# Optimization experiments

Measured on AMD Instinct MI355X. Metric: run time of the kernel, lower is better.

## Reference

```python
import jax, jax.numpy as jnp
import numpy as np

D_MODEL = 2048
NUM_HEADS = 16
D_K = D_MODEL // NUM_HEADS


def setup_inputs() -> dict:
    key = jax.random.key(0)
    ks = jax.random.split(key, 12)
    B, S, D = 2, 2048, D_MODEL
    s = 1.0 / np.sqrt(D)
    return {
        "q": jax.random.normal(ks[0], (B, S, D), jnp.float32),
        "k": jax.random.normal(ks[1], (B, S, D), jnp.float32),
        "v": jax.random.normal(ks[2], (B, S, D), jnp.float32),
        "Wq": jax.random.normal(ks[3], (D, D), jnp.float32) * s,
        "bq": jax.random.normal(ks[4], (D,), jnp.float32) * 0.01,
        "Wk": jax.random.normal(ks[5], (D, D), jnp.float32) * s,
        "bk": jax.random.normal(ks[6], (D,), jnp.float32) * 0.01,
        "Wv": jax.random.normal(ks[7], (D, D), jnp.float32) * s,
        "bv": jax.random.normal(ks[8], (D,), jnp.float32) * 0.01,
        "Wo": jax.random.normal(ks[9], (D, D), jnp.float32) * s,
        "bo": jax.random.normal(ks[10], (D,), jnp.float32) * 0.01,
    }


def reference(q, k, v, Wq, bq, Wk, bk, Wv, bv, Wo, bo):
    B, S, D = q.shape
    H, dk = NUM_HEADS, D_K

    def proj(x, W, b):
        # Linear then split heads -> [B, H, S, dk]
        y = jnp.einsum('bsd,df->bsf', x, W) + b
        return y.reshape(B, -1, H, dk).transpose(0, 2, 1, 3)

    Q = proj(q, Wq, bq)
    K = proj(k, Wk, bk)
    V = proj(v, Wv, bv)

    scores = jnp.einsum('bhqd,bhkd->bhqk', Q, K) / jnp.sqrt(jnp.float32(dk))
    attn = jax.nn.softmax(scores, axis=-1)  # dropout is identity (eval)
    out = jnp.einsum('bhqk,bhkd->bhqd', attn, V)
    out = out.transpose(0, 2, 1, 3).reshape(B, -1, D)
    return jnp.einsum('bsd,df->bsf', out, Wo) + bo
```

## Files before the change

kernel.cpp:

```cpp
#include <hip/hip_runtime.h>
#include <hip/hip_bf16.h>
#include <stdint.h>

typedef float  f32x4  __attribute__((ext_vector_type(4)));
typedef float  f32x16 __attribute__((ext_vector_type(16)));
typedef short  s16x8  __attribute__((ext_vector_type(8)));

#define D_MODEL 2048
#define NHEADS  16
#define DK      128
#define BATCH   2
#define SEQ     2048
#define MROWS   (BATCH*SEQ)

__device__ __forceinline__ unsigned short f2bf(float f) {
  union { float f; unsigned int u; } v; v.f = f;
  unsigned int r = v.u + 0x7FFFu + ((v.u >> 16) & 1u);
  return (unsigned short)(r >> 16);
}

__device__ __forceinline__ unsigned int packbf(float lo, float hi) {
  return (unsigned int)f2bf(lo) | ((unsigned int)f2bf(hi) << 16);
}

__device__ __forceinline__ unsigned int packbf_c(float lo, float hi) {
  __hip_bfloat16 l = __float2bfloat16(lo);
  __hip_bfloat16 h = __float2bfloat16(hi);
  unsigned short lu, hu;
  __builtin_memcpy(&lu, &l, 2);
  __builtin_memcpy(&hu, &h, 2);
  return (unsigned int)lu | ((unsigned int)hu << 16);
}

__device__ __forceinline__ void async16(const void* g, void* l) {
  __builtin_amdgcn_global_load_lds(
      (const __attribute__((address_space(1))) unsigned int*)g,
      (__attribute__((address_space(3))) unsigned int*)l,
      16, 0, 0);
}

__global__ __launch_bounds__(256) void f2b3_kernel(const float* __restrict__ q,
                                                   const float* __restrict__ k,
                                                   const float* __restrict__ v,
                                                   unsigned short* __restrict__ qb,
                                                   unsigned short* __restrict__ kb,
                                                   unsigned short* __restrict__ vb) {
  const float* s; unsigned short* d;
  switch (blockIdx.y) {
    case 0:  s = q; d = qb; break;
    case 1:  s = k; d = kb; break;
    default: s = v; d = vb; break;
  }
  int i = blockIdx.x * 256 + threadIdx.x;
  const float4* s4 = (const float4*)s;
  float4 a = s4[2*i];
  float4 b = s4[2*i+1];
  s16x8 o;
  o[0] = (short)f2bf(a.x); o[1] = (short)f2bf(a.y);
  o[2] = (short)f2bf(a.z); o[3] = (short)f2bf(a.w);
  o[4] = (short)f2bf(b.x); o[5] = (short)f2bf(b.y);
  o[6] = (short)f2bf(b.z); o[7] = (short)f2bf(b.w);
  *(s16x8*)(d + 8*(size_t)i) = o;
}

__global__ __launch_bounds__(256) void wtrans_kernel(const float* __restrict__ Wq,
                                                     const float* __restrict__ Wk,
                                                     const float* __restrict__ Wv,
                                                     const float* __restrict__ Wo,
                                                     unsigned short* __restrict__ WqT,
                                                     unsigned short* __restrict__ WkT,
                                                     unsigned short* __restrict__ WvT,
                                                     unsigned short* __restrict__ WoT) {
  const float* W; unsigned short* Wt;
  switch (blockIdx.z) {
    case 0:  W = Wq; Wt = WqT; break;
    case 1:  W = Wk; Wt = WkT; break;
    case 2:  W = Wv; Wt = WvT; break;
    default: W = Wo; Wt = WoT; break;
  }
  __shared__ float tl[32][33];
  int x = threadIdx.x, y = threadIdx.y;
  int n0 = blockIdx.x * 32, k0 = blockIdx.y * 32;
  #pragma unroll
  for (int j = 0; j < 32; j += 8)
    tl[y + j][x] = W[(size_t)(k0 + y + j) * D_MODEL + n0 + x];
  __syncthreads();
  #pragma unroll
  for (int j = 0; j < 32; j += 8)
    Wt[(size_t)(n0 + y + j) * D_MODEL + k0 + x] = f2bf(tl[x][y + j]);
}

__global__ __launch_bounds__(256) void gemm_bt(const unsigned short* __restrict__ A,
                                               const unsigned short* __restrict__ Bt,
                                               const float* __restrict__ bias,
                                               void* __restrict__ Cout,
                                               int M, int N, int K,
                                               int mode, float scale) {
  __shared__ unsigned short As[128*32];
  __shared__ unsigned short Bs[128*32];
  const int t  = threadIdx.x;
  const int l  = t & 63, w = t >> 6;
  const int wr = w >> 1, wc = w & 1;
  const int m0 = blockIdx.y * 128, n0 = blockIdx.x * 128;
  const int lr = l & 15, lg = l >> 4;

  f32x4 acc[4][4] = {};

  for (int k0 = 0; k0 < K; k0 += 32) {
    __syncthreads();
    #pragma unroll
    for (int i = 0; i < 2; ++i) {
      int c    = t + 256*i;
      int row  = c >> 2;
      int col8 = (c & 3) * 8;
      async16(A  + (size_t)(m0 + row)*K + k0 + col8, (char*)As + c*16);
      async16(Bt + (size_t)(n0 + row)*K + k0 + col8, (char*)Bs + c*16);
    }
    asm volatile("s_waitcnt vmcnt(0)" ::: "memory");
    __syncthreads();

    s16x8 af[4], bfr[4];
    #pragma unroll
    for (int m = 0; m < 4; ++m)
      af[m] = *(const s16x8*)&As[(wr*64 + m*16 + lr)*32 + 8*lg];
    #pragma unroll
    for (int n = 0; n < 4; ++n)
      bfr[n] = *(const s16x8*)&Bs[(wc*64 + n*16 + lr)*32 + 8*lg];
    #pragma unroll
    for (int m = 0; m < 4; ++m)
      #pragma unroll
      for (int n = 0; n < 4; ++n)
        acc[m][n] = __builtin_amdgcn_mfma_f32_16x16x32_bf16(af[m], bfr[n], acc[m][n], 0, 0, 0);
  }

  if (mode == 0) {
    float* C = (float*)Cout;
    #pragma unroll
    for (int n = 0; n < 4; ++n) {
      int col = n0 + wc*64 + n*16 + lr;
      float bv = bias[col];
      #pragma unroll
      for (int m = 0; m < 4; ++m) {
        int rowb = m0 + wr*64 + m*16 + lg*4;
        #pragma unroll
        for (int r = 0; r < 4; ++r)
          C[(size_t)(rowb + r)*N + col] = (acc[m][n][r] + bv) * scale;
      }
    }
  } else {
    unsigned short* C = (unsigned short*)Cout;
    #pragma unroll
    for (int n = 0; n < 4; ++n) {
      int col = n0 + wc*64 + n*16 + lr;
      float bv = bias[col];
      int h = col >> 7, dkk = col & 127;
      #pragma unroll
      for (int m = 0; m < 4; ++m) {
        int rowb = m0 + wr*64 + m*16 + lg*4;
        #pragma unroll
        for (int r = 0; r < 4; ++r) {
          int row = rowb + r;
          int b = row >> 11, s = row & 2047;
          C[((size_t)((b*NHEADS + h)*SEQ + s))*DK + dkk] = f2bf((acc[m][n][r] + bv) * scale);
        }
      }
    }
  }
}

__global__ __launch_bounds__(256, 2) void attn_kernel(const unsigned short* __restrict__ Q,
                                                      const unsigned short* __restrict__ K,
                                                      const unsigned short* __restrict__ V,
                                                      unsigned short* __restrict__ O) {
  #define BUFSZ (64*256 + 128*144)
  __shared__ char lds[2*BUFSZ];

  const int t  = threadIdx.x;
  const int l  = t & 63, w = t >> 6;
  const int q_ = l & 31, hi = l >> 5;
  const int bh = blockIdx.y;
  const int b  = bh >> 4, h = bh & 15;
  const int q0 = blockIdx.x * 128;

  const unsigned short* Qp = Q + (size_t)bh * SEQ * DK;
  const unsigned short* Kp = K + (size_t)bh * SEQ * DK;
  const unsigned short* Vp = V + (size_t)bh * SEQ * DK;

  const int qrow = q0 + w*32 + q_;
  s16x8 aq[8];
  #pragma unroll
  for (int kk = 0; kk < 8; ++kk)
    aq[kk] = *(const s16x8*)(Qp + (size_t)qrow*DK + kk*16 + hi*8);

  f32x16 accO[4] = {};
  float m = -INFINITY, L = 0.f;

  const int vp_ = t & 31;
  const int vd0 = (t >> 5) * 8;

  s16x8 va0, vb0, va1, vb1;

  {
    char* KlN = lds;
    #pragma unroll
    for (int i = 0; i < 4; ++i) {
      int c   = t + 256*i;
      int row = c >> 4;
      int sb  = ((c & 15) << 4) ^ ((row & 15) << 4);
      async16((const char*)(Kp + (size_t)row*DK) + sb, KlN + c*16);
    }
    va0 = *(const s16x8*)(Vp + (size_t)(2*vp_    )*DK + vd0);
    vb0 = *(const s16x8*)(Vp + (size_t)(2*vp_ + 1)*DK + vd0);
    va1 = *(const s16x8*)(Vp + (size_t)(2*vp_    )*DK + vd0 + 64);
    vb1 = *(const s16x8*)(Vp + (size_t)(2*vp_ + 1)*DK + vd0 + 64);
  }

  for (int tt = 0; tt < SEQ/64; ++tt) {
    char*           Kl = lds + (tt & 1)*BUFSZ;
    unsigned short* Vt = (unsigned short*)(Kl + 64*256);

    asm volatile("s_waitcnt vmcnt(0)" ::: "memory");
    #pragma unroll
    for (int j = 0; j < 8; ++j) {
      unsigned int pk0 = (unsigned int)(unsigned short)va0[j]
                       | ((unsigned int)(unsigned short)vb0[j] << 16);
      *(unsigned int*)&Vt[(vd0 + j)*72 + 2*vp_] = pk0;
      unsigned int pk1 = (unsigned int)(unsigned short)va1[j]
                       | ((unsigned int)(unsigned short)vb1[j] << 16);
      *(unsigned int*)&Vt[(vd0 + 64 + j)*72 + 2*vp_] = pk1;
    }
    asm volatile("s_waitcnt lgkmcnt(0)" ::: "memory");
    __syncthreads();

    if (tt + 1 < SEQ/64) {
      int   kvn = (tt + 1) * 64;
      char* KlN = lds + ((tt & 1) ^ 1)*BUFSZ;
      #pragma unroll
      for (int i = 0; i < 4; ++i) {
        int c   = t + 256*i;
        int row = c >> 4;
        int sb  = ((c & 15) << 4) ^ ((row & 15) << 4);
        async16((const char*)(Kp + (size_t)(kvn + row)*DK) + sb, KlN + c*16);
      }
      va0 = *(const s16x8*)(Vp + (size_t)(kvn + 2*vp_    )*DK + vd0);
      vb0 = *(const s16x8*)(Vp + (size_t)(kvn + 2*vp_ + 1)*DK + vd0);
      va1 = *(const s16x8*)(Vp + (size_t)(kvn + 2*vp_    )*DK + vd0 + 64);
      vb1 = *(const s16x8*)(Vp + (size_t)(kvn + 2*vp_ + 1)*DK + vd0 + 64);
    }

    f32x16 S0 = {}, S1 = {};
    #pragma unroll
    for (int t2 = 0; t2 < 2; ++t2) {
      int krow = t2*32 + q_;
      const char* kb = Kl + krow*256;
      int swz = (krow & 15) << 4;
      #pragma unroll
      for (int kk = 0; kk < 8; ++kk) {
        s16x8 kf = *(const s16x8*)(kb + ((kk*32 + hi*16) ^ swz));
        if (t2 == 0) S0 = __builtin_amdgcn_mfma_f32_32x32x16_bf16(kf, aq[kk], S0, 0, 0, 0);
        else         S1 = __builtin_amdgcn_mfma_f32_32x32x16_bf16(kf, aq[kk], S1, 0, 0, 0);
      }
    }

    f32x16 mx;
    #pragma unroll
    for (int r = 0; r < 16; ++r) mx[r] = fmaxf(S0[r], S1[r]);
    float m8_[8];
    #pragma unroll
    for (int r = 0; r < 8; ++r) m8_[r] = fmaxf(mx[r], mx[r+8]);
    float m4a = fmaxf(m8_[0], m8_[4]), m4b = fmaxf(m8_[1], m8_[5]);
    float m4c = fmaxf(m8_[2], m8_[6]), m4d = fmaxf(m8_[3], m8_[7]);
    float pmax = fmaxf(fmaxf(m4a, m4b), fmaxf(m4c, m4d));
    pmax = fmaxf(pmax, __shfl_xor(pmax, 32, 64));

    if (!__all(pmax <= m + 11.0f)) {
      float mnew = fmaxf(m, pmax);
      float corr = exp2f(m - mnew);
      m = mnew;
      L *= corr;
      #pragma unroll
      for (int sub = 0; sub < 4; ++sub)
        #pragma unroll
        for (int r = 0; r < 16; ++r) accO[sub][r] *= corr;
    }

    float rs0 = 0.f, rs1 = 0.f, rs2 = 0.f, rs3 = 0.f;
    #pragma unroll
    for (int r = 0; r < 4; ++r) {
      float a0 = exp2f(S0[r]    - m); S0[r]    = a0; rs0 += a0;
      float a1 = exp2f(S0[r+4]  - m); S0[r+4]  = a1; rs1 += a1;
      float a2 = exp2f(S0[r+8]  - m); S0[r+8]  = a2; rs2 += a2;
      float a3 = exp2f(S0[r+12] - m); S0[r+12] = a3; rs3 += a3;
      float b0 = exp2f(S1[r]    - m); S1[r]    = b0; rs0 += b0;
      float b1 = exp2f(S1[r+4]  - m); S1[r+4]  = b1; rs1 += b1;
      float b2 = exp2f(S1[r+8]  - m); S1[r+8]  = b2; rs2 += b2;
      float b3 = exp2f(S1[r+12] - m); S1[r+12] = b3; rs3 += b3;
    }
    float rs = (rs0 + rs1) + (rs2 + rs3);
    rs += __shfl_xor(rs, 32, 64);
    L += rs;

    s16x8 PB[4];
    #pragma unroll
    for (int t2 = 0; t2 < 2; ++t2) {
      #pragma unroll
      for (int half = 0; half < 2; ++half) {
        int bse = half*8;
        unsigned int pkA01, pkA23, pkB01, pkB23;
        if (t2 == 0) {
          pkA01 = packbf_c(S0[bse+0], S0[bse+1]);
          pkA23 = packbf_c(S0[bse+2], S0[bse+3]);
          pkB01 = packbf_c(S0[bse+4], S0[bse+5]);
          pkB23 = packbf_c(S0[bse+6], S0[bse+7]);
        } else {
          pkA01 = packbf_c(S1[bse+0], S1[bse+1]);
          pkA23 = packbf_c(S1[bse+2], S1[bse+3]);
          pkB01 = packbf_c(S1[bse+4], S1[bse+5]);
          pkB23 = packbf_c(S1[bse+6], S1[bse+7]);
        }
        unsigned int xA01 = __shfl_xor(pkA01, 32, 64);
        unsigned int xA23 = __shfl_xor(pkA23, 32, 64);
        unsigned int xB01 = __shfl_xor(pkB01, 32, 64);
        unsigned int xB23 = __shfl_xor(pkB23, 32, 64);
        union { unsigned int u[4]; s16x8 v; } f;
        f.u[0] = hi ? xB01 : pkA01;
        f.u[1] = hi ? xB23 : pkA23;
        f.u[2] = hi ? pkB01 : xA01;
        f.u[3] = hi ? pkB23 : xA23;
        PB[t2*2 + half] = f.v;
      }
    }

    #pragma unroll
    for (int sub = 0; sub < 4; ++sub) {
      const char* vb2 = (const char*)Vt + (size_t)(sub*32 + q_)*144 + hi*16;
      #pragma unroll
      for (int kk = 0; kk < 4; ++kk) {
        s16x8 vf = *(const s16x8*)(vb2 + kk*32);
        accO[sub] = __builtin_amdgcn_mfma_f32_32x32x16_bf16(vf, PB[kk], accO[sub], 0, 0, 0);
      }
    }
  }

  __syncthreads();
  unsigned short* Ob = (unsigned short*)lds + (size_t)w*4096;
  float inv = 1.0f / L;
  #pragma unroll
  for (int sub = 0; sub < 4; ++sub)
    #pragma unroll
    for (int j = 0; j < 8; ++j) {
      unsigned int pw = packbf_c(accO[sub][2*j]*inv, accO[sub][2*j+1]*inv);
      int dv = sub*32 + (j&1)*2 + ((j>>1)*8) + 4*hi;
      *(unsigned int*)((char*)Ob + q_*256 + ((dv*2) ^ ((q_ & 15) << 4))) = pw;
    }
  asm volatile("s_waitcnt lgkmcnt(0)" ::: "memory");
  size_t gbase = ((size_t)(b*SEQ + q0 + w*32 + q_))*D_MODEL + h*DK;
  #pragma unroll
  for (int p = 0; p < 8; ++p) {
    int chunk = hi + 2*p;
    s16x8 ov = *(const s16x8*)((char*)Ob + q_*256 + ((chunk*16) ^ ((q_ & 15) << 4)));
    *(s16x8*)(O + gbase + chunk*8) = ov;
  }
  #undef BUFSZ
}

extern "C" void kernel_launch(void* const* d_in, const int* in_sizes, int n_in,
                              void* d_out, int out_size, void* d_ws, size_t ws_size,
                              hipStream_t stream) {
  const float* q  = (const float*)d_in[0];
  const float* k  = (const float*)d_in[1];
  const float* v  = (const float*)d_in[2];
  const float* Wq = (const float*)d_in[3];
  const float* bq = (const float*)d_in[4];
  const float* Wk = (const float*)d_in[5];
  const float* bk = (const float*)d_in[6];
  const float* Wv = (const float*)d_in[7];
  const float* bv = (const float*)d_in[8];
  const float* Wo = (const float*)d_in[9];
  const float* bo = (const float*)d_in[10];
  float* out = (float*)d_out;

  char* ws = (char*)d_ws;
  const size_t SZT = (size_t)MROWS * D_MODEL * 2;
  const size_t SZW = (size_t)D_MODEL * D_MODEL * 2;

  unsigned short* qb  = (unsigned short*)(ws);
  unsigned short* kb  = (unsigned short*)(ws + SZT);
  unsigned short* vb  = (unsigned short*)(ws + 2*SZT);
  unsigned short* WqT = (unsigned short*)(ws + 3*SZT);
  unsigned short* WkT = (unsigned short*)(ws + 3*SZT + SZW);
  unsigned short* WvT = (unsigned short*)(ws + 3*SZT + 2*SZW);
  unsigned short* WoT = (unsigned short*)(ws + 3*SZT + 3*SZW);
  unsigned short* Qh  = (unsigned short*)(ws + 3*SZT + 4*SZW);
  unsigned short* Kh  = (unsigned short*)(ws + 4*SZT + 4*SZW);
  unsigned short* Vh  = (unsigned short*)(ws + 5*SZT + 4*SZW);
  unsigned short* Oc  = qb;

  const int n8 = MROWS * D_MODEL / 8;
  f2b3_kernel<<<dim3(n8/256, 3), 256, 0, stream>>>(q, k, v, qb, kb, vb);
  wtrans_kernel<<<dim3(64, 64, 4), dim3(32, 8), 0, stream>>>(Wq, Wk, Wv, Wo, WqT, WkT, WvT, WoT);

  const float qscale = 0.1275174308f;
  gemm_bt<<<dim3(16, 32), 256, 0, stream>>>(qb, WqT, bq, Qh, MROWS, D_MODEL, D_MODEL, 1, qscale);
  gemm_bt<<<dim3(16, 32), 256, 0, stream>>>(kb, WkT, bk, Kh, MROWS, D_MODEL, D_MODEL, 1, 1.0f);
  gemm_bt<<<dim3(16, 32), 256, 0, stream>>>(vb, WvT, bv, Vh, MROWS, D_MODEL, D_MODEL, 1, 1.0f);

  attn_kernel<<<dim3(SEQ/128, BATCH*NHEADS), 256, 0, stream>>>(Qh, Kh, Vh, Oc);

  gemm_bt<<<dim3(16, 32), 256, 0, stream>>>(Oc, WoT, bo, out, MROWS, D_MODEL, D_MODEL, 0, 1.0f);
}
```

Measured before the change: 374.5 us.

## Double-buffer GEMM tiles; single-buffer attention K/V for higher occupancy

The projection GEMM now double-buffers its A/B LDS tiles, issuing the async loads for the next K-slice before computing the current one, so global loads overlap the MFMAs. The attention kernel moves the other way: it drops its double-buffered K/V staging for a single buffer and raises its launch bound from 2 to 4 blocks per CU, relying on occupancy rather than in-kernel prefetch to hide latency. This trades explicit overlap in attention for more resident waves, which may help or hurt depending on register pressure and LDS limits.

```diff
diff --git a/kernel.cpp b/kernel.cpp
--- a/kernel.cpp
+++ b/kernel.cpp
@@ -17,10 +17,6 @@
   union { float f; unsigned int u; } v; v.f = f;
   unsigned int r = v.u + 0x7FFFu + ((v.u >> 16) & 1u);
   return (unsigned short)(r >> 16);
-}
-
-__device__ __forceinline__ unsigned int packbf(float lo, float hi) {
-  return (unsigned int)f2bf(lo) | ((unsigned int)f2bf(hi) << 16);
 }
 
 __device__ __forceinline__ unsigned int packbf_c(float lo, float hi) {
@@ -96,41 +92,51 @@
                                                void* __restrict__ Cout,
                                                int M, int N, int K,
                                                int mode, float scale) {
-  __shared__ unsigned short As[128*32];
-  __shared__ unsigned short Bs[128*32];
+  __shared__ unsigned short As[2][128*32];
+  __shared__ unsigned short Bs[2][128*32];
   const int t  = threadIdx.x;
   const int l  = t & 63, w = t >> 6;
   const int wr = w >> 1, wc = w & 1;
   const int m0 = blockIdx.y * 128, n0 = blockIdx.x * 128;
   const int lr = l & 15, lg = l >> 4;
 
+  const int c0row = t >> 2, c0col = (t & 3) * 8;
+  const int c1row = (t + 256) >> 2, c1col = ((t + 256) & 3) * 8;
+
+  async16(A  + (size_t)(m0 + c0row)*K + c0col, (char*)As[0] + t*16);
+  async16(Bt + (size_t)(n0 + c0row)*K + c0col, (char*)Bs[0] + t*16);
+  async16(A  + (size_t)(m0 + c1row)*K + c1col, (char*)As[0] + (t+256)*16);
+  async16(Bt + (size_t)(n0 + c1row)*K + c1col, (char*)Bs[0] + (t+256)*16);
+  asm volatile("s_waitcnt vmcnt(0)" ::: "memory");
+  __syncthreads();
+
   f32x4 acc[4][4] = {};
 
   for (int k0 = 0; k0 < K; k0 += 32) {
-    __syncthreads();
-    #pragma unroll
-    for (int i = 0; i < 2; ++i) {
-      int c    = t + 256*i;
-      int row  = c >> 2;
-      int col8 = (c & 3) * 8;
-      async16(A  + (size_t)(m0 + row)*K + k0 + col8, (char*)As + c*16);
-      async16(Bt + (size_t)(n0 + row)*K + k0 + col8, (char*)Bs + c*16);
-    }
+    const int cur = (k0 >> 5) & 1;
+    if (k0 + 32 < K) {
+      const int kn = k0 + 32;
+      async16(A  + (size_t)(m0 + c0row)*K + kn + c0col, (char*)As[cur^1] + t*16);
+      async16(Bt + (size_t)(n0 + c0row)*K + kn + c0col, (char*)Bs[cur^1] + t*16);
+      async16(A  + (size_t)(m0 + c1row)*K + kn + c1col, (char*)As[cur^1] + (t+256)*16);
+      async16(Bt + (size_t)(n0 + c1row)*K + kn + c1col, (char*)Bs[cur^1] + (t+256)*16);
+    }
+
+    s16x8 af[4], bfr[4];
+    #pragma unroll
+    for (int m = 0; m < 4; ++m)
+      af[m] = *(const s16x8*)&As[cur][(wr*64 + m*16 + lr)*32 + 8*lg];
+    #pragma unroll
+    for (int n = 0; n < 4; ++n)
+      bfr[n] = *(const s16x8*)&Bs[cur][(wc*64 + n*16 + lr)*32 + 8*lg];
+    #pragma unroll
+    for (int m = 0; m < 4; ++m)
+      #pragma unroll
+      for (int n = 0; n < 4; ++n)
+        acc[m][n] = __builtin_amdgcn_mfma_f32_16x16x32_bf16(af[m], bfr[n], acc[m][n], 0, 0, 0);
+
     asm volatile("s_waitcnt vmcnt(0)" ::: "memory");
     __syncthreads();
-
-    s16x8 af[4], bfr[4];
-    #pragma unroll
-    for (int m = 0; m < 4; ++m)
-      af[m] = *(const s16x8*)&As[(wr*64 + m*16 + lr)*32 + 8*lg];
-    #pragma unroll
-    for (int n = 0; n < 4; ++n)
-      bfr[n] = *(const s16x8*)&Bs[(wc*64 + n*16 + lr)*32 + 8*lg];
-    #pragma unroll
-    for (int m = 0; m < 4; ++m)
-      #pragma unroll
-      for (int n = 0; n < 4; ++n)
-        acc[m][n] = __builtin_amdgcn_mfma_f32_16x16x32_bf16(af[m], bfr[n], acc[m][n], 0, 0, 0);
   }
 
   if (mode == 0) {
@@ -168,12 +174,13 @@
   }
 }
 
-__global__ __launch_bounds__(256, 2) void attn_kernel(const unsigned short* __restrict__ Q,
+__global__ __launch_bounds__(256, 4) void attn_kernel(const unsigned short* __restrict__ Q,
                                                       const unsigned short* __restrict__ K,
                                                       const unsigned short* __restrict__ V,
                                                       unsigned short* __restrict__ O) {
-  #define BUFSZ (64*256 + 128*144)
-  __shared__ char lds[2*BUFSZ];
+  __shared__ char lds[64*256 + 128*144];
+  unsigned short* Kl = (unsigned short*)lds;
+  unsigned short* Vt = (unsigned short*)(lds + 64*256);
 
   const int t  = threadIdx.x;
   const int l  = t & 63, w = t >> 6;
@@ -198,61 +205,35 @@
   const int vp_ = t & 31;
   const int vd0 = (t >> 5) * 8;
 
-  s16x8 va0, vb0, va1, vb1;
-
-  {
-    char* KlN = lds;
+  for (int kv0 = 0; kv0 < SEQ; kv0 += 64) {
+    __syncthreads();
     #pragma unroll
     for (int i = 0; i < 4; ++i) {
       int c   = t + 256*i;
       int row = c >> 4;
       int sb  = ((c & 15) << 4) ^ ((row & 15) << 4);
-      async16((const char*)(Kp + (size_t)row*DK) + sb, KlN + c*16);
-    }
-    va0 = *(const s16x8*)(Vp + (size_t)(2*vp_    )*DK + vd0);
-    vb0 = *(const s16x8*)(Vp + (size_t)(2*vp_ + 1)*DK + vd0);
-    va1 = *(const s16x8*)(Vp + (size_t)(2*vp_    )*DK + vd0 + 64);
-    vb1 = *(const s16x8*)(Vp + (size_t)(2*vp_ + 1)*DK + vd0 + 64);
-  }
-
-  for (int tt = 0; tt < SEQ/64; ++tt) {
-    char*           Kl = lds + (tt & 1)*BUFSZ;
-    unsigned short* Vt = (unsigned short*)(Kl + 64*256);
-
-    asm volatile("s_waitcnt vmcnt(0)" ::: "memory");
-    #pragma unroll
-    for (int j = 0; j < 8; ++j) {
-      unsigned int pk0 = (unsigned int)(unsigned short)va0[j]
-                       | ((unsigned int)(unsigned short)vb0[j] << 16);
-      *(unsigned int*)&Vt[(vd0 + j)*72 + 2*vp_] = pk0;
-      unsigned int pk1 = (unsigned int)(unsigned short)va1[j]
-                       | ((unsigned int)(unsigned short)vb1[j] << 16);
-      *(unsigned int*)&Vt[(vd0 + 64 + j)*72 + 2*vp_] = pk1;
-    }
-    asm volatile("s_waitcnt lgkmcnt(0)" ::: "memory");
+      async16((const char*)(Kp + (size_t)(kv0 + row)*DK) + sb, (char*)Kl + c*16);
+    }
+    #pragma unroll
+    for (int rep = 0; rep < 2; ++rep) {
+      int dvb = vd0 + rep*64;
+      s16x8 va = *(const s16x8*)(Vp + (size_t)(kv0 + 2*vp_    )*DK + dvb);
+      s16x8 vb = *(const s16x8*)(Vp + (size_t)(kv0 + 2*vp_ + 1)*DK + dvb);
+      #pragma unroll
+      for (int j = 0; j < 8; ++j) {
+        unsigned int pk = (unsigned int)(unsigned short)va[j]
+                        | ((unsigned int)(unsigned short)vb[j] << 16);
+        *(unsigned int*)&Vt[(dvb + j)*72 + 2*vp_] = pk;
+      }
+    }
+    asm volatile("s_waitcnt vmcnt(0) lgkmcnt(0)" ::: "memory");
     __syncthreads();
-
-    if (tt + 1 < SEQ/64) {
-      int   kvn = (tt + 1) * 64;
-      char* KlN = lds + ((tt & 1) ^ 1)*BUFSZ;
-      #pragma unroll
-      for (int i = 0; i < 4; ++i) {
-        int c   = t + 256*i;
-        int row = c >> 4;
-        int sb  = ((c & 15) << 4) ^ ((row & 15) << 4);
-        async16((const char*)(Kp + (size_t)(kvn + row)*DK) + sb, KlN + c*16);
-      }
-      va0 = *(const s16x8*)(Vp + (size_t)(kvn + 2*vp_    )*DK + vd0);
-      vb0 = *(const s16x8*)(Vp + (size_t)(kvn + 2*vp_ + 1)*DK + vd0);
-      va1 = *(const s16x8*)(Vp + (size_t)(kvn + 2*vp_    )*DK + vd0 + 64);
-      vb1 = *(const s16x8*)(Vp + (size_t)(kvn + 2*vp_ + 1)*DK + vd0 + 64);
-    }
 
     f32x16 S0 = {}, S1 = {};
     #pragma unroll
     for (int t2 = 0; t2 < 2; ++t2) {
       int krow = t2*32 + q_;
-      const char* kb = Kl + krow*256;
+      const char* kb = (const char*)Kl + krow*256;
       int swz = (krow & 15) << 4;
       #pragma unroll
       for (int kk = 0; kk < 8; ++kk) {
@@ -361,7 +342,6 @@
     s16x8 ov = *(const s16x8*)((char*)Ob + q_*256 + ((chunk*16) ^ ((q_ & 15) << 4)));
     *(s16x8*)(O + gbase + chunk*8) = ov;
   }
-  #undef BUFSZ
 }
 
 extern "C" void kernel_launch(void* const* d_in, const int* in_sizes, int n_in,
```

Result: slower. 521.7 us (+39.3%).
